# Optimization experiments

Measured on AMD Instinct MI355X. Metric: run time of the kernel, lower is better.

Reference implementation:

```python
import jax, jax.numpy as jnp
import numpy as np

N_NODES = 17   # fixed by Linear(256, 17) + residual add
D = 512        # feature dim
H = 8          # number of attention heads


def setup_inputs() -> dict:
    key = jax.random.key(0)
    ks = jax.random.split(key, 8)
    return {
        "Xs": jax.random.normal(ks[0], (N_NODES, D), dtype=jnp.float32),
        "ROIs_b": jax.random.uniform(ks[1], (N_NODES, 3), dtype=jnp.float32),
        "adj": jnp.zeros((N_NODES, N_NODES), dtype=jnp.float32),  # unused in forward
        "FC": jax.random.normal(ks[2], (H, D, D), dtype=jnp.float32) * (1.414 / np.sqrt(D)),
        "W1": jax.random.normal(ks[3], (H, D + 3, 256), dtype=jnp.float32) * (1.0 / np.sqrt(D + 3)),
        "b1": jnp.zeros((H, 256), dtype=jnp.float32),
        "W2": jax.random.normal(ks[4], (H, 256, N_NODES), dtype=jnp.float32) * (1.0 / np.sqrt(256)),
        "b2": jnp.zeros((H, N_NODES), dtype=jnp.float32),
        "conv_w": jax.random.normal(ks[5], (H,), dtype=jnp.float32) * 0.3,
        "conv_b": jnp.zeros((1,), dtype=jnp.float32),
    }


def reference(Xs, ROIs_b, adj, FC, W1, b1, W2, b2, conv_w, conv_b):
    # All 8 heads batched over leading axis h (original launches them as
    # separate Python-level modules).
    # f_input = relu(Xs @ FC) per head: [H, N, D]
    f = jax.nn.relu(jnp.einsum('nd,hde->hne', Xs, FC))
    # concat coordinates: [H, N, D+3]
    coords = jnp.broadcast_to(ROIs_b[None], (f.shape[0], ROIs_b.shape[0], ROIs_b.shape[1]))
    cat = jnp.concatenate([f, coords], axis=-1)
    # 2-layer MLP: Linear(515,256) -> tanh -> Linear(256,17): [H, N, 17]
    hdn = jnp.tanh(jnp.einsum('hnc,hcm->hnm', cat, W1) + b1[:, None, :])
    att = jnp.einsum('hnm,hmk->hnk', hdn, W2) + b2[:, None, :]
    # permute(1,0) then softmax over dim=1 (the N axis): [H, 17, N]
    att = jax.nn.softmax(jnp.swapaxes(att, 1, 2), axis=-1)
    # weighted sum over nodes: [H, 17, D]
    h_prime = jnp.einsum('hkn,hnd->hkd', att, f)
    # Conv1d(8,1,1) over head axis + ReLU, then residual
    out = jax.nn.relu(jnp.einsum('h,hkd->kd', conv_w, h_prime) + conv_b[0])
    Xs_out = out + Xs  # [17, 512]
    # original returns a list of per-landmark views [1,512,1,1,1]; we return
    # the equivalent stacked array plus passthrough ROIs
    return Xs_out, ROIs_b
```

## Files before the change

kernel.cpp:

```cpp
#include <hip/hip_runtime.h>

#define NN 17
#define D  512
#define H  8
#define C1 515
#define M  256

#define XPAD 20
#define RSN  36
#define RSG  (NN * RSN)
#define SMEM_FL (32 * RSG)

__device__ __forceinline__ void fma4(float4& a, float x, const float4& w) {
    a.x = fmaf(x, w.x, a.x); a.y = fmaf(x, w.y, a.y);
    a.z = fmaf(x, w.z, a.z); a.w = fmaf(x, w.w, a.w);
}

__global__ __launch_bounds__(256) void k1_f(const float* __restrict__ Xs,
                                            const float* __restrict__ FC,
                                            float* __restrict__ f) {
    const int b = blockIdx.x;
    const int et = b & 15, h = b >> 4;
    const int t = threadIdx.x, tw = t & 7, cg = t >> 3;
    __shared__ float sm[SMEM_FL];
    for (int i = t; i < NN * D; i += 256) {
        const int n = i >> 9, d = i & 511;
        sm[d * XPAD + n] = Xs[i];
    }
    __syncthreads();
    float4 acc[NN];
#pragma unroll
    for (int n = 0; n < NN; ++n) acc[n] = make_float4(0.f, 0.f, 0.f, 0.f);
    const float4* fc4 = (const float4*)(FC + (size_t)h * D * D) + et * 8 + tw;
#pragma unroll 4
    for (int i = 0; i < 16; ++i) {
        const int d = cg + (i << 5);
        const float4 w = fc4[d << 7];
        const float* xr = sm + d * XPAD;
#pragma unroll
        for (int n4 = 0; n4 < 4; ++n4) {
            const float4 x = *(const float4*)(xr + (n4 << 2));
            fma4(acc[n4 * 4 + 0], x.x, w);
            fma4(acc[n4 * 4 + 1], x.y, w);
            fma4(acc[n4 * 4 + 2], x.z, w);
            fma4(acc[n4 * 4 + 3], x.w, w);
        }
        fma4(acc[16], xr[16], w);
    }
    __syncthreads();
    float* rr = sm + cg * RSG + tw * 4;
#pragma unroll
    for (int n = 0; n < NN; ++n) *(float4*)(rr + n * RSN) = acc[n];
    __syncthreads();
    for (int i = t; i < NN * 32; i += 256) {
        const int n = i >> 5, e = i & 31;
        float s = 0.f;
#pragma unroll 8
        for (int g = 0; g < 32; ++g) s += sm[g * RSG + n * RSN + e];
        f[((h * NN + n) << 9) + (et << 5) + e] = fmaxf(s, 0.f);
    }
}

__global__ __launch_bounds__(256) void k2_hdn(const float* __restrict__ f,
                                              const float* __restrict__ ROIs,
                                              const float* __restrict__ W1,
                                              const float* __restrict__ b1,
                                              float* __restrict__ hdn) {
    const int b = blockIdx.x;
    const int mt = b & 7, h = b >> 3;
    const int t = threadIdx.x, tw = t & 7, cg = t >> 3;
    __shared__ float sm[SMEM_FL];
    for (int i = t; i < NN * D; i += 256) {
        const int n = i >> 9, d = i & 511;
        sm[d * XPAD + n] = f[((size_t)(h * NN) << 9) + i];
    }
    if (t < NN * 3) {
        const int n = t / 3, cc = t % 3;
        sm[(D + cc) * XPAD + n] = ROIs[t];
    }
    __syncthreads();
    float4 acc[NN];
#pragma unroll
    for (int n = 0; n < NN; ++n) acc[n] = make_float4(0.f, 0.f, 0.f, 0.f);
    const float4* w4 = (const float4*)(W1 + (size_t)h * C1 * M) + mt * 8 + tw;
#pragma unroll 4
    for (int i = 0; i < 16; ++i) {
        const int c = cg + (i << 5);
        const float4 w = w4[c << 6];
        const float* xr = sm + c * XPAD;
#pragma unroll
        for (int n4 = 0; n4 < 4; ++n4) {
            const float4 x = *(const float4*)(xr + (n4 << 2));
            fma4(acc[n4 * 4 + 0], x.x, w);
            fma4(acc[n4 * 4 + 1], x.y, w);
            fma4(acc[n4 * 4 + 2], x.z, w);
            fma4(acc[n4 * 4 + 3], x.w, w);
        }
        fma4(acc[16], xr[16], w);
    }
    if (cg < 3) {
        const int c = D + cg;
        const float4 w = w4[c << 6];
        const float* xr = sm + c * XPAD;
#pragma unroll
        for (int n4 = 0; n4 < 4; ++n4) {
            const float4 x = *(const float4*)(xr + (n4 << 2));
            fma4(acc[n4 * 4 + 0], x.x, w);
            fma4(acc[n4 * 4 + 1], x.y, w);
            fma4(acc[n4 * 4 + 2], x.z, w);
            fma4(acc[n4 * 4 + 3], x.w, w);
        }
        fma4(acc[16], xr[16], w);
    }
    __syncthreads();
    float* rr = sm + cg * RSG + tw * 4;
#pragma unroll
    for (int n = 0; n < NN; ++n) *(float4*)(rr + n * RSN) = acc[n];
    __syncthreads();
    for (int i = t; i < NN * 32; i += 256) {
        const int n = i >> 5, m = i & 31;
        float s = b1[h * M + (mt << 5) + m];
#pragma unroll 8
        for (int g = 0; g < 32; ++g) s += sm[g * RSG + n * RSN + m];
        hdn[(h * NN + n) * M + (mt << 5) + m] = tanhf(s);
    }
}

__global__ __launch_bounds__(256) void k34(const float* __restrict__ hdn,
                                           const float* __restrict__ W2,
                                           const float* __restrict__ b2,
                                           const float* __restrict__ f,
                                           const float* __restrict__ conv_w,
                                           const float* __restrict__ conv_b,
                                           const float* __restrict__ Xs,
                                           const float* __restrict__ ROIs,
                                           float* __restrict__ out) {
    const int k = blockIdx.x, t = threadIdx.x;
    __shared__ float swk[H][M + 4];
    __shared__ float sa[H][NN];
    __shared__ float cw[H];
    for (int i = t; i < H * M; i += 256) {
        const int h = i >> 8, m = i & 255;
        swk[h][m] = W2[(size_t)(h * M + m) * NN + k];
    }
    if (t < H) cw[t] = conv_w[t];
    __syncthreads();
    if (t < H * NN) {
        const int h = t / NN, n = t % NN;
        const float4* a4 = (const float4*)(hdn + (h * NN + n) * M);
        const float4* w4 = (const float4*)(&swk[h][0]);
        float acc = b2[h * NN + k];
#pragma unroll 8
        for (int m4 = 0; m4 < M / 4; ++m4) {
            const float4 av = a4[m4];
            const float4 wv = w4[m4];
            acc = fmaf(av.x, wv.x, acc); acc = fmaf(av.y, wv.y, acc);
            acc = fmaf(av.z, wv.z, acc); acc = fmaf(av.w, wv.w, acc);
        }
        sa[h][n] = acc;
    }
    __syncthreads();
    if (t < H) {
        float mx = -1e30f;
#pragma unroll
        for (int n = 0; n < NN; ++n) mx = fmaxf(mx, sa[t][n]);
        float e[NN];
        float s = 0.f;
#pragma unroll
        for (int n = 0; n < NN; ++n) { e[n] = __expf(sa[t][n] - mx); s += e[n]; }
        const float inv = 1.f / s;
#pragma unroll
        for (int n = 0; n < NN; ++n) sa[t][n] = e[n] * inv;
    }
    __syncthreads();
    const float cb = conv_b[0];
    float acc0 = 0.f, acc1 = 0.f;
    for (int h = 0; h < H; ++h) {
        float w0 = 0.f, w1 = 0.f;
#pragma unroll
        for (int n = 0; n < NN; ++n) {
            const float a = sa[h][n];
            const float* fr = f + (size_t)((h * NN + n) << 9);
            w0 = fmaf(a, fr[t], w0);
            w1 = fmaf(a, fr[t + 256], w1);
        }
        acc0 = fmaf(cw[h], w0, acc0);
        acc1 = fmaf(cw[h], w1, acc1);
    }
    out[(k << 9) + t]       = fmaxf(acc0 + cb, 0.f) + Xs[(k << 9) + t];
    out[(k << 9) + t + 256] = fmaxf(acc1 + cb, 0.f) + Xs[(k << 9) + t + 256];
    if (k == 0 && t < NN * 3) out[NN * D + t] = ROIs[t];
}

extern "C" void kernel_launch(void* const* d_in, const int* in_sizes, int n_in,
                              void* d_out, int out_size, void* d_ws, size_t ws_size,
                              hipStream_t stream) {
    const float* Xs     = (const float*)d_in[0];
    const float* ROIs   = (const float*)d_in[1];
    const float* FC     = (const float*)d_in[3];
    const float* W1     = (const float*)d_in[4];
    const float* b1     = (const float*)d_in[5];
    const float* W2     = (const float*)d_in[6];
    const float* b2     = (const float*)d_in[7];
    const float* conv_w = (const float*)d_in[8];
    const float* conv_b = (const float*)d_in[9];
    float* out = (float*)d_out;

    float* f   = (float*)d_ws;
    float* hdn = f + H * NN * D;

    k1_f  <<<H * 16, 256, 0, stream>>>(Xs, FC, f);
    k2_hdn<<<H * 8,  256, 0, stream>>>(f, ROIs, W1, b1, hdn);
    k34   <<<NN,     256, 0, stream>>>(hdn, W2, b2, f, conv_w, conv_b, Xs, ROIs, out);
}
```

Baseline: 109.1 us.

## Fuse three kernels into one persistent launch with software grid barriers

Merges the three stage kernels into a single 128-block kernel and separates the stages with atomic-counter grid barriers, with a memset clearing the counters before each launch. This removes two kernel launch boundaries and their inter-kernel gaps. In exchange, idle blocks spin at the barriers and a memset is added per call. Correctness depends on all 128 blocks being co-resident.

Measured after the change: 146.5 us. +34.3%, slower.

```diff
diff --git a/kernel.cpp b/kernel.cpp
--- a/kernel.cpp
+++ b/kernel.cpp
@@ -6,6 +6,8 @@
 #define C1 515
 #define M  256
 
+#define NBLOCKS 128
+
 #define XPAD 20
 #define RSN  36
 #define RSG  (NN * RSN)
@@ -16,180 +18,190 @@
     a.z = fmaf(x, w.z, a.z); a.w = fmaf(x, w.w, a.w);
 }
 
-__global__ __launch_bounds__(256) void k1_f(const float* __restrict__ Xs,
-                                            const float* __restrict__ FC,
-                                            float* __restrict__ f) {
+__device__ __forceinline__ void grid_barrier(unsigned int* ctr, unsigned int nb) {
+    __threadfence();
+    __syncthreads();
+    if (threadIdx.x == 0) {
+        atomicAdd(ctr, 1u);
+        while (__hip_atomic_load(ctr, __ATOMIC_RELAXED, __HIP_MEMORY_SCOPE_AGENT) < nb) {
+            __builtin_amdgcn_s_sleep(8);
+        }
+    }
+    __syncthreads();
+    __threadfence();
+}
+
+__global__ __launch_bounds__(256) void fused_all(
+        const float* __restrict__ Xs,     const float* __restrict__ ROIs,
+        const float* __restrict__ FC,     const float* __restrict__ W1,
+        const float* __restrict__ b1,     const float* __restrict__ W2,
+        const float* __restrict__ b2,     const float* __restrict__ conv_w,
+        const float* __restrict__ conv_b, float* __restrict__ out,
+        float* __restrict__ f,            float* __restrict__ hdn,
+        unsigned int* __restrict__ ctrs) {
     const int b = blockIdx.x;
-    const int et = b & 15, h = b >> 4;
-    const int t = threadIdx.x, tw = t & 7, cg = t >> 3;
-    __shared__ float sm[SMEM_FL];
-    for (int i = t; i < NN * D; i += 256) {
-        const int n = i >> 9, d = i & 511;
-        sm[d * XPAD + n] = Xs[i];
-    }
-    __syncthreads();
-    float4 acc[NN];
-#pragma unroll
-    for (int n = 0; n < NN; ++n) acc[n] = make_float4(0.f, 0.f, 0.f, 0.f);
-    const float4* fc4 = (const float4*)(FC + (size_t)h * D * D) + et * 8 + tw;
+    const int t = threadIdx.x;
+    __shared__ __align__(16) float sm[SMEM_FL];
+
+    {
+        const int et = b & 15, h = b >> 4;
+        const int tw = t & 7, cgr = t >> 3;
+        for (int i = t; i < NN * D; i += 256) {
+            const int n = i >> 9, d = i & 511;
+            sm[d * XPAD + n] = Xs[i];
+        }
+        __syncthreads();
+        float4 acc[NN];
+#pragma unroll
+        for (int n = 0; n < NN; ++n) acc[n] = make_float4(0.f, 0.f, 0.f, 0.f);
+        const float4* fc4 = (const float4*)(FC + (size_t)h * D * D) + et * 8 + tw;
 #pragma unroll 4
-    for (int i = 0; i < 16; ++i) {
-        const int d = cg + (i << 5);
-        const float4 w = fc4[d << 7];
-        const float* xr = sm + d * XPAD;
-#pragma unroll
-        for (int n4 = 0; n4 < 4; ++n4) {
-            const float4 x = *(const float4*)(xr + (n4 << 2));
-            fma4(acc[n4 * 4 + 0], x.x, w);
-            fma4(acc[n4 * 4 + 1], x.y, w);
-            fma4(acc[n4 * 4 + 2], x.z, w);
-            fma4(acc[n4 * 4 + 3], x.w, w);
-        }
-        fma4(acc[16], xr[16], w);
-    }
-    __syncthreads();
-    float* rr = sm + cg * RSG + tw * 4;
-#pragma unroll
-    for (int n = 0; n < NN; ++n) *(float4*)(rr + n * RSN) = acc[n];
-    __syncthreads();
-    for (int i = t; i < NN * 32; i += 256) {
-        const int n = i >> 5, e = i & 31;
-        float s = 0.f;
+        for (int i = 0; i < 16; ++i) {
+            const int d = cgr + (i << 5);
+            const float4 w = fc4[d << 7];
+            const float* xr = sm + d * XPAD;
+#pragma unroll
+            for (int n4 = 0; n4 < 4; ++n4) {
+                const float4 x = *(const float4*)(xr + (n4 << 2));
+                fma4(acc[n4 * 4 + 0], x.x, w);
+                fma4(acc[n4 * 4 + 1], x.y, w);
+                fma4(acc[n4 * 4 + 2], x.z, w);
+                fma4(acc[n4 * 4 + 3], x.w, w);
+            }
+            fma4(acc[16], xr[16], w);
+        }
+        __syncthreads();
+        float* rr = sm + cgr * RSG + tw * 4;
+#pragma unroll
+        for (int n = 0; n < NN; ++n) *(float4*)(rr + n * RSN) = acc[n];
+        __syncthreads();
+        for (int i = t; i < NN * 32; i += 256) {
+            const int n = i >> 5, e = i & 31;
+            float s = 0.f;
 #pragma unroll 8
-        for (int g = 0; g < 32; ++g) s += sm[g * RSG + n * RSN + e];
-        f[((h * NN + n) << 9) + (et << 5) + e] = fmaxf(s, 0.f);
-    }
-}
-
-__global__ __launch_bounds__(256) void k2_hdn(const float* __restrict__ f,
-                                              const float* __restrict__ ROIs,
-                                              const float* __restrict__ W1,
-                                              const float* __restrict__ b1,
-                                              float* __restrict__ hdn) {
-    const int b = blockIdx.x;
-    const int mt = b & 7, h = b >> 3;
-    const int t = threadIdx.x, tw = t & 7, cg = t >> 3;
-    __shared__ float sm[SMEM_FL];
-    for (int i = t; i < NN * D; i += 256) {
-        const int n = i >> 9, d = i & 511;
-        sm[d * XPAD + n] = f[((size_t)(h * NN) << 9) + i];
-    }
-    if (t < NN * 3) {
-        const int n = t / 3, cc = t % 3;
-        sm[(D + cc) * XPAD + n] = ROIs[t];
-    }
-    __syncthreads();
-    float4 acc[NN];
-#pragma unroll
-    for (int n = 0; n < NN; ++n) acc[n] = make_float4(0.f, 0.f, 0.f, 0.f);
-    const float4* w4 = (const float4*)(W1 + (size_t)h * C1 * M) + mt * 8 + tw;
+            for (int g = 0; g < 32; ++g) s += sm[g * RSG + n * RSN + e];
+            f[((h * NN + n) << 9) + (et << 5) + e] = fmaxf(s, 0.f);
+        }
+    }
+    grid_barrier(ctrs + 0, NBLOCKS);
+
+    if (b < H * 8) {
+        const int mt = b & 7, h = b >> 3;
+        const int tw = t & 7, cgr = t >> 3;
+        for (int i = t; i < NN * D; i += 256) {
+            const int n = i >> 9, d = i & 511;
+            sm[d * XPAD + n] = f[((size_t)(h * NN) << 9) + i];
+        }
+        if (t < NN * 3) {
+            const int n = t / 3, cc = t % 3;
+            sm[(D + cc) * XPAD + n] = ROIs[t];
+        }
+        __syncthreads();
+        float4 acc[NN];
+#pragma unroll
+        for (int n = 0; n < NN; ++n) acc[n] = make_float4(0.f, 0.f, 0.f, 0.f);
+        const float4* w4 = (const float4*)(W1 + (size_t)h * C1 * M) + mt * 8 + tw;
 #pragma unroll 4
-    for (int i = 0; i < 16; ++i) {
-        const int c = cg + (i << 5);
-        const float4 w = w4[c << 6];
-        const float* xr = sm + c * XPAD;
-#pragma unroll
-        for (int n4 = 0; n4 < 4; ++n4) {
-            const float4 x = *(const float4*)(xr + (n4 << 2));
-            fma4(acc[n4 * 4 + 0], x.x, w);
-            fma4(acc[n4 * 4 + 1], x.y, w);
-            fma4(acc[n4 * 4 + 2], x.z, w);
-            fma4(acc[n4 * 4 + 3], x.w, w);
-        }
-        fma4(acc[16], xr[16], w);
-    }
-    if (cg < 3) {
-        const int c = D + cg;
-        const float4 w = w4[c << 6];
-        const float* xr = sm + c * XPAD;
-#pragma unroll
-        for (int n4 = 0; n4 < 4; ++n4) {
-            const float4 x = *(const float4*)(xr + (n4 << 2));
-            fma4(acc[n4 * 4 + 0], x.x, w);
-            fma4(acc[n4 * 4 + 1], x.y, w);
-            fma4(acc[n4 * 4 + 2], x.z, w);
-            fma4(acc[n4 * 4 + 3], x.w, w);
-        }
-        fma4(acc[16], xr[16], w);
-    }
-    __syncthreads();
-    float* rr = sm + cg * RSG + tw * 4;
-#pragma unroll
-    for (int n = 0; n < NN; ++n) *(float4*)(rr + n * RSN) = acc[n];
-    __syncthreads();
-    for (int i = t; i < NN * 32; i += 256) {
-        const int n = i >> 5, m = i & 31;
-        float s = b1[h * M + (mt << 5) + m];
+        for (int i = 0; i < 16; ++i) {
+            const int c = cgr + (i << 5);
+            const float4 w = w4[c << 6];
+            const float* xr = sm + c * XPAD;
+#pragma unroll
+            for (int n4 = 0; n4 < 4; ++n4) {
+                const float4 x = *(const float4*)(xr + (n4 << 2));
+                fma4(acc[n4 * 4 + 0], x.x, w);
+                fma4(acc[n4 * 4 + 1], x.y, w);
+                fma4(acc[n4 * 4 + 2], x.z, w);
+                fma4(acc[n4 * 4 + 3], x.w, w);
+            }
+            fma4(acc[16], xr[16], w);
+        }
+        if (cgr < 3) {
+            const int c = D + cgr;
+            const float4 w = w4[c << 6];
+            const float* xr = sm + c * XPAD;
+#pragma unroll
+            for (int n4 = 0; n4 < 4; ++n4) {
+                const float4 x = *(const float4*)(xr + (n4 << 2));
+                fma4(acc[n4 * 4 + 0], x.x, w);
+                fma4(acc[n4 * 4 + 1], x.y, w);
+                fma4(acc[n4 * 4 + 2], x.z, w);
+                fma4(acc[n4 * 4 + 3], x.w, w);
+            }
+            fma4(acc[16], xr[16], w);
+        }
+        __syncthreads();
+        float* rr = sm + cgr * RSG + tw * 4;
+#pragma unroll
+        for (int n = 0; n < NN; ++n) *(float4*)(rr + n * RSN) = acc[n];
+        __syncthreads();
+        for (int i = t; i < NN * 32; i += 256) {
+            const int n = i >> 5, m = i & 31;
+            float s = b1[h * M + (mt << 5) + m];
 #pragma unroll 8
-        for (int g = 0; g < 32; ++g) s += sm[g * RSG + n * RSN + m];
-        hdn[(h * NN + n) * M + (mt << 5) + m] = tanhf(s);
-    }
-}
-
-__global__ __launch_bounds__(256) void k34(const float* __restrict__ hdn,
-                                           const float* __restrict__ W2,
-                                           const float* __restrict__ b2,
-                                           const float* __restrict__ f,
-                                           const float* __restrict__ conv_w,
-                                           const float* __restrict__ conv_b,
-                                           const float* __restrict__ Xs,
-                                           const float* __restrict__ ROIs,
-                                           float* __restrict__ out) {
-    const int k = blockIdx.x, t = threadIdx.x;
-    __shared__ float swk[H][M + 4];
-    __shared__ float sa[H][NN];
-    __shared__ float cw[H];
-    for (int i = t; i < H * M; i += 256) {
-        const int h = i >> 8, m = i & 255;
-        swk[h][m] = W2[(size_t)(h * M + m) * NN + k];
-    }
-    if (t < H) cw[t] = conv_w[t];
-    __syncthreads();
-    if (t < H * NN) {
-        const int h = t / NN, n = t % NN;
-        const float4* a4 = (const float4*)(hdn + (h * NN + n) * M);
-        const float4* w4 = (const float4*)(&swk[h][0]);
-        float acc = b2[h * NN + k];
+            for (int g = 0; g < 32; ++g) s += sm[g * RSG + n * RSN + m];
+            hdn[(h * NN + n) * M + (mt << 5) + m] = tanhf(s);
+        }
+    }
+    grid_barrier(ctrs + 32, NBLOCKS);
+
+    if (b < NN) {
+        const int k = b;
+        float* swk = sm;
+        float* sa  = sm + H * (M + 4);
+        float* cwv = sm + H * (M + 4) + H * NN;
+        for (int i = t; i < H * M; i += 256) {
+            const int h = i >> 8, m = i & 255;
+            swk[h * (M + 4) + m] = W2[(size_t)(h * M + m) * NN + k];
+        }
+        if (t < H) cwv[t] = conv_w[t];
+        __syncthreads();
+        if (t < H * NN) {
+            const int h = t / NN, n = t % NN;
+            const float4* a4 = (const float4*)(hdn + (h * NN + n) * M);
+            const float4* w4 = (const float4*)(swk + h * (M + 4));
+            float acc = b2[h * NN + k];
 #pragma unroll 8
-        for (int m4 = 0; m4 < M / 4; ++m4) {
-            const float4 av = a4[m4];
-            const float4 wv = w4[m4];
-            acc = fmaf(av.x, wv.x, acc); acc = fmaf(av.y, wv.y, acc);
-            acc = fmaf(av.z, wv.z, acc); acc = fmaf(av.w, wv.w, acc);
-        }
-        sa[h][n] = acc;
-    }
-    __syncthreads();
-    if (t < H) {
-        float mx = -1e30f;
-#pragma unroll
-        for (int n = 0; n < NN; ++n) mx = fmaxf(mx, sa[t][n]);
-        float e[NN];
-        float s = 0.f;
-#pragma unroll
-        for (int n = 0; n < NN; ++n) { e[n] = __expf(sa[t][n] - mx); s += e[n]; }
-        const float inv = 1.f / s;
-#pragma unroll
-        for (int n = 0; n < NN; ++n) sa[t][n] = e[n] * inv;
-    }
-    __syncthreads();
-    const float cb = conv_b[0];
-    float acc0 = 0.f, acc1 = 0.f;
-    for (int h = 0; h < H; ++h) {
-        float w0 = 0.f, w1 = 0.f;
-#pragma unroll
-        for (int n = 0; n < NN; ++n) {
-            const float a = sa[h][n];
-            const float* fr = f + (size_t)((h * NN + n) << 9);
-            w0 = fmaf(a, fr[t], w0);
-            w1 = fmaf(a, fr[t + 256], w1);
-        }
-        acc0 = fmaf(cw[h], w0, acc0);
-        acc1 = fmaf(cw[h], w1, acc1);
-    }
-    out[(k << 9) + t]       = fmaxf(acc0 + cb, 0.f) + Xs[(k << 9) + t];
-    out[(k << 9) + t + 256] = fmaxf(acc1 + cb, 0.f) + Xs[(k << 9) + t + 256];
-    if (k == 0 && t < NN * 3) out[NN * D + t] = ROIs[t];
+            for (int m4 = 0; m4 < M / 4; ++m4) {
+                const float4 av = a4[m4];
+                const float4 wv = w4[m4];
+                acc = fmaf(av.x, wv.x, acc); acc = fmaf(av.y, wv.y, acc);
+                acc = fmaf(av.z, wv.z, acc); acc = fmaf(av.w, wv.w, acc);
+            }
+            sa[h * NN + n] = acc;
+        }
+        __syncthreads();
+        if (t < H) {
+            float mx = -1e30f;
+#pragma unroll
+            for (int n = 0; n < NN; ++n) mx = fmaxf(mx, sa[t * NN + n]);
+            float e[NN];
+            float s = 0.f;
+#pragma unroll
+            for (int n = 0; n < NN; ++n) { e[n] = __expf(sa[t * NN + n] - mx); s += e[n]; }
+            const float inv = 1.f / s;
+#pragma unroll
+            for (int n = 0; n < NN; ++n) sa[t * NN + n] = e[n] * inv;
+        }
+        __syncthreads();
+        const float cb = conv_b[0];
+        float acc0 = 0.f, acc1 = 0.f;
+        for (int h = 0; h < H; ++h) {
+            float w0 = 0.f, w1 = 0.f;
+#pragma unroll
+            for (int n = 0; n < NN; ++n) {
+                const float a = sa[h * NN + n];
+                const float* fr = f + (size_t)((h * NN + n) << 9);
+                w0 = fmaf(a, fr[t], w0);
+                w1 = fmaf(a, fr[t + 256], w1);
+            }
+            acc0 = fmaf(cwv[h], w0, acc0);
+            acc1 = fmaf(cwv[h], w1, acc1);
+        }
+        out[(k << 9) + t]       = fmaxf(acc0 + cb, 0.f) + Xs[(k << 9) + t];
+        out[(k << 9) + t + 256] = fmaxf(acc1 + cb, 0.f) + Xs[(k << 9) + t + 256];
+        if (k == 0 && t < NN * 3) out[NN * D + t] = ROIs[t];
+    }
 }
 
 extern "C" void kernel_launch(void* const* d_in, const int* in_sizes, int n_in,
@@ -204,12 +216,15 @@
     const float* b2     = (const float*)d_in[7];
     const float* conv_w = (const float*)d_in[8];
     const float* conv_b = (const float*)d_in[9];
-    float* out = (float*)d_out;
-
-    float* f   = (float*)d_ws;
-    float* hdn = f + H * NN * D;
-
-    k1_f  <<<H * 16, 256, 0, stream>>>(Xs, FC, f);
-    k2_hdn<<<H * 8,  256, 0, stream>>>(f, ROIs, W1, b1, hdn);
-    k34   <<<NN,     256, 0, stream>>>(hdn, W2, b2, f, conv_w, conv_b, Xs, ROIs, out);
-}
+    float* outp = (float*)d_out;
+
+    float* fbuf   = (float*)d_ws;
+    float* hdnbuf = fbuf + H * NN * D;
+
+    unsigned int* ctrs = (unsigned int*)((char*)d_ws + (1u << 20));
+    hipMemsetAsync(ctrs, 0, 256, stream);
+
+    fused_all<<<NBLOCKS, 256, 0, stream>>>(Xs, ROIs, FC, W1, b1, W2, b2,
+                                           conv_w, conv_b, outp, fbuf, hdnbuf,
+                                           ctrs);
+}
```
